# Optimization experiments

Hardware: AMD Instinct MI355X
Metric: run time of the kernel (lower is better)

## Reference

```python
import jax, jax.numpy as jnp
import numpy as np


def setup_inputs() -> dict:
    key = jax.random.key(0)
    ks = jax.random.split(key, 7)
    B = 4096
    x = jax.random.normal(ks[0], (B, 1, 28, 28), dtype=jnp.float32)
    # conv1: Conv2d(1, 32, 3), conv2: Conv2d(32, 64, 3)
    w1 = jax.random.normal(ks[1], (32, 1, 3, 3), dtype=jnp.float32) * 0.1
    b1 = jax.random.normal(ks[2], (32,), dtype=jnp.float32) * 0.1
    w2 = jax.random.normal(ks[3], (64, 32, 3, 3), dtype=jnp.float32) * 0.05
    b2 = jax.random.normal(ks[4], (64,), dtype=jnp.float32) * 0.05
    # fc1: Linear(9216, 128), fc2: Linear(128, 10)
    fc1_w = jax.random.normal(ks[5], (128, 9216), dtype=jnp.float32) * 0.01
    fc1_b = jnp.zeros((128,), dtype=jnp.float32)
    fc2_w = jax.random.normal(ks[6], (10, 128), dtype=jnp.float32) * 0.05
    fc2_b = jnp.zeros((10,), dtype=jnp.float32)
    return {"x": x, "w1": w1, "b1": b1, "w2": w2, "b2": b2,
            "fc1_w": fc1_w, "fc1_b": fc1_b, "fc2_w": fc2_w, "fc2_b": fc2_b}


def _conv_valid(x, w, b):
    # The original FFTConv1d (flatten-to-1D FFT circular correlation + roll +
    # crop) is mathematically identical to valid cross-correlation (nn.Conv2d).
    y = jax.lax.conv_general_dilated(
        x, w, window_strides=(1, 1), padding="VALID",
        dimension_numbers=("NCHW", "OIHW", "NCHW"))
    return y + b[None, :, None, None]


def reference(x, w1, b1, w2, b2, fc1_w, fc1_b, fc2_w, fc2_b):
    h = jax.nn.relu(_conv_valid(x, w1, b1))        # [B,32,26,26]
    h = jax.nn.relu(_conv_valid(h, w2, b2))        # [B,64,24,24]
    B, C, H, W = h.shape
    h = h.reshape(B, C, H // 2, 2, W // 2, 2).max(axis=(3, 5))  # maxpool 2x2 -> [B,64,12,12]
    # dropout layers are identity at inference
    h = h.reshape(B, -1)                           # [B,9216], C-major like torch.flatten
    h = jax.nn.relu(h @ fc1_w.T + fc1_b)           # [B,128]
    logits = h @ fc2_w.T + fc2_b                   # [B,10]
    # original computes log_softmax but returns the pre-softmax logits
    return logits
```

## Files before the change

### kernel.cpp

```cpp
#include <hip/hip_runtime.h>
#include <hip/hip_bf16.h>
#include <string.h>

using short8 = __attribute__((ext_vector_type(8))) short;
using f32x4  = __attribute__((ext_vector_type(4))) float;

#define POOLN     9216
#define FC1N      128
#define WT2_ELEMS 18432
#define WT2_BYTES 36864
#define H1S_STRIDE 36
#define XS_STRIDE  29

#define GLL16(gp, lp) __builtin_amdgcn_global_load_lds( \
    (const __attribute__((address_space(1))) void*)(gp), \
    (__attribute__((address_space(3))) void*)(lp), 16, 0, 0)

static __device__ __forceinline__ unsigned short f2bf(float f) {
  unsigned int u = __builtin_bit_cast(unsigned int, f);
  unsigned int r = (u + 0x7FFFu + ((u >> 16) & 1u)) >> 16;
  return (unsigned short)r;
}

static __device__ __forceinline__ unsigned int pkbf(float lo, float hi) {
  __hip_bfloat162 h2 = __float22bfloat162_rn(make_float2(lo, hi));
  unsigned int r;
  memcpy(&r, &h2, sizeof(r));
  return r;
}

__global__ __launch_bounds__(256) void k_wt2(const float* __restrict__ w2,
    unsigned short* __restrict__ wt2) {
  int idx = blockIdx.x * 256 + threadIdx.x;
  if (idx >= WT2_ELEMS) return;
  int j = idx & 7;
  int l = (idx >> 3) & 63;
  int tn = idx >> 9;
  int tap = tn >> 2, n = tn & 3;
  int oc = n * 16 + (l & 15);
  int ic = (l >> 4) * 8 + j;
  wt2[idx] = f2bf(w2[oc * 288 + ic * 9 + tap]);
}

__global__ __launch_bounds__(256) void k_fw1t(const float* __restrict__ w,
    unsigned short* __restrict__ wt) {
  int c = blockIdx.x;
  __shared__ float row[9216];
  int t = threadIdx.x;
  const float* src = w + (size_t)c * 9216;
  for (int i = t; i < 9216; i += 256) row[i] = src[i];
  __syncthreads();
  unsigned short* dst = wt + (size_t)c * 9216;
  for (int k = t; k < 9216; k += 256) {
    int sp = k >> 6, oc = k & 63;
    dst[k] = f2bf(row[oc * 144 + sp]);
  }
}

__global__ __launch_bounds__(256, 3) void kc_fused(const float* __restrict__ x,
    const float* __restrict__ w1, const float* __restrict__ b1,
    const unsigned short* __restrict__ wt2, const float* __restrict__ b2,
    unsigned short* __restrict__ pooled) {
  int img = blockIdx.x;
  int tt = blockIdx.y;
  __shared__ float xs[12 * XS_STRIDE];
  __shared__ __align__(16) unsigned short h1s[260 * H1S_STRIDE];
  int t = threadIdx.x;
  int wv = t >> 6, ln = t & 63;
  int r0x = tt * 8;

  const float* xp = x + (size_t)img * 784 + (size_t)r0x * 28;
  for (int i = t; i < 12 * 28; i += 256) {
    int r = i / 28, c = i - r * 28;
    xs[r * XS_STRIDE + c] = xp[r * 28 + c];
  }

  int wvu = __builtin_amdgcn_readfirstlane(wv);
  float wr[8][9], br[8];
  #pragma unroll
  for (int o = 0; o < 8; ++o) {
    br[o] = b1[wvu * 8 + o];
    #pragma unroll
    for (int q = 0; q < 9; ++q) wr[o][q] = w1[(wvu * 8 + o) * 9 + q];
  }
  __syncthreads();

  if (ln < 52) {
    int half = (ln >= 26);
    int xcol = ln - half * 26;
    int y0 = half * 5;
    float win[3][3];
    #pragma unroll
    for (int c = 0; c < 3; ++c) {
      win[1][c] = xs[(y0 + 0) * XS_STRIDE + xcol + c];
      win[2][c] = xs[(y0 + 1) * XS_STRIDE + xcol + c];
    }
    #pragma unroll
    for (int i = 0; i < 5; ++i) {
      #pragma unroll
      for (int c = 0; c < 3; ++c) {
        win[0][c] = win[1][c];
        win[1][c] = win[2][c];
        win[2][c] = xs[(y0 + i + 2) * XS_STRIDE + xcol + c];
      }
      unsigned int packed[4];
      #pragma unroll
      for (int o = 0; o < 8; o += 2) {
        float s0 = br[o], s1 = br[o + 1];
        #pragma unroll
        for (int r = 0; r < 3; ++r)
          #pragma unroll
          for (int c = 0; c < 3; ++c) {
            s0 = fmaf(win[r][c], wr[o][r * 3 + c], s0);
            s1 = fmaf(win[r][c], wr[o + 1][r * 3 + c], s1);
          }
        packed[o >> 1] = pkbf(fmaxf(s0, 0.f), fmaxf(s1, 0.f));
      }
      int pos = (y0 + i) * 26 + xcol;
      unsigned short* dst = &h1s[pos * H1S_STRIDE + wv * 8];
      *(uint2*)dst = make_uint2(packed[0], packed[1]);
      *(uint2*)(dst + 4) = make_uint2(packed[2], packed[3]);
    }
  }
  __syncthreads();

  int col = ln & 15;
  int g = (ln >> 4) & 3;

  int abase[3];
  #pragma unroll
  for (int i = 0; i < 3; ++i) {
    int y = 2 * wv + (col & 1);
    int xx = 8 * i + (col >> 1);
    abase[i] = (y * 26 + xx) * (H1S_STRIDE * 2) + g * 16;
  }

  f32x4 acc[3][4];
  #pragma unroll
  for (int m = 0; m < 3; ++m)
    #pragma unroll
    for (int n = 0; n < 4; ++n)
      acc[m][n] = (f32x4){0.f, 0.f, 0.f, 0.f};

  const char* hsb = (const char*)h1s;
  #pragma unroll
  for (int tap = 0; tap < 9; ++tap) {
    int ky = tap / 3, kx = tap - ky * 3;
    int toff = (ky * 26 + kx) * (H1S_STRIDE * 2);
    short8 bf[4];
    #pragma unroll
    for (int n = 0; n < 4; ++n)
      bf[n] = *(const short8*)(wt2 + ((size_t)(tap * 4 + n) * 64 + ln) * 8);
    #pragma unroll
    for (int m = 0; m < 3; ++m) {
      union { short8 v; uint2 d[2]; } af;
      af.d[0] = *(const uint2*)(hsb + abase[m] + toff);
      af.d[1] = *(const uint2*)(hsb + abase[m] + toff + 8);
      #pragma unroll
      for (int n = 0; n < 4; ++n)
        acc[m][n] = __builtin_amdgcn_mfma_f32_16x16x32_bf16(af.v, bf[n], acc[m][n], 0, 0, 0);
    }
  }

  float bias[4];
  #pragma unroll
  for (int n = 0; n < 4; ++n) bias[n] = b2[n * 16 + col];
  unsigned short* pp = pooled + (size_t)img * POOLN;
  int pr = tt * 4 + wv;
  #pragma unroll
  for (int m = 0; m < 3; ++m) {
    int sp = pr * 12 + m * 4 + g;
    float rv[4];
    #pragma unroll
    for (int n = 0; n < 4; ++n) {
      f32x4 a = acc[m][n];
      float v = fmaxf(fmaxf(a[0], a[1]), fmaxf(a[2], a[3]));
      rv[n] = fmaxf(v + bias[n], 0.f);
    }
    unsigned int p01 = pkbf(rv[0], rv[1]);
    unsigned int p23 = pkbf(rv[2], rv[3]);
    unsigned short* pr0 = pp + sp * 64 + col;
    pr0[0]  = (unsigned short)p01;
    pr0[16] = (unsigned short)(p01 >> 16);
    pr0[32] = (unsigned short)p23;
    pr0[48] = (unsigned short)(p23 >> 16);
  }
}

__global__ __launch_bounds__(256) void k3_fc1_mfma(
    const unsigned short* __restrict__ a, const unsigned short* __restrict__ w,
    float* __restrict__ part, int nrpad) {
  __shared__ __align__(16) unsigned short As[2][4096];
  __shared__ __align__(16) unsigned short Bs[2][8192];
  int row0 = blockIdx.x * 64;
  int kbase = blockIdx.y * 2304;
  int t = threadIdx.x;
  int wv = t >> 6, l = t & 63;
  int rsub = l >> 3;
  int src_sw = ((l & 7) ^ rsub) << 4;

  const char* abase = (const char*)a + (size_t)row0 * 18432;
  const char* bbase = (const char*)w;

  auto stage = [&](int buf, int step) {
    size_t k0b = (size_t)(kbase + step * 64) * 2;
    #pragma unroll
    for (int i = 0; i < 2; ++i) {
      int c = wv * 2 + i;
      GLL16(abase + (size_t)(c * 8 + rsub) * 18432 + k0b + src_sw,
            (char*)As[buf] + c * 1024);
    }
    #pragma unroll
    for (int i = 0; i < 4; ++i) {
      int c = wv * 4 + i;
      GLL16(bbase + (size_t)(c * 8 + rsub) * 18432 + k0b + src_sw,
            (char*)Bs[buf] + c * 1024);
    }
  };

  int wm = wv >> 1, wn = wv & 1;
  int lr = l & 15, g2 = l >> 4;
  int rdxor = (lr & 7) << 4;

  f32x4 acc[2][4];
  #pragma unroll
  for (int mf = 0; mf < 2; ++mf)
    #pragma unroll
    for (int nf = 0; nf < 4; ++nf)
      acc[mf][nf] = (f32x4){0.f, 0.f, 0.f, 0.f};

  stage(0, 0);
  __syncthreads();
  for (int s = 0; s < 36; ++s) {
    int cur = s & 1;
    if (s < 35) stage(cur ^ 1, s + 1);
    const char* Ab = (const char*)As[cur];
    const char* Bb = (const char*)Bs[cur];
    #pragma unroll
    for (int ksub = 0; ksub < 2; ++ksub) {
      int koff = (ksub * 64 + g2 * 16) ^ rdxor;
      short8 af0 = *(const short8*)(Ab + (wm * 32 + lr) * 128 + koff);
      short8 af1 = *(const short8*)(Ab + (wm * 32 + 16 + lr) * 128 + koff);
      short8 bf[4];
      #pragma unroll
      for (int nf = 0; nf < 4; ++nf)
        bf[nf] = *(const short8*)(Bb + (wn * 64 + nf * 16 + lr) * 128 + koff);
      #pragma unroll
      for (int nf = 0; nf < 4; ++nf) {
        acc[0][nf] = __builtin_amdgcn_mfma_f32_16x16x32_bf16(af0, bf[nf], acc[0][nf], 0, 0, 0);
        acc[1][nf] = __builtin_amdgcn_mfma_f32_16x16x32_bf16(af1, bf[nf], acc[1][nf], 0, 0, 0);
      }
    }
    __syncthreads();
  }

  float* pp = part + (size_t)blockIdx.y * nrpad * 128 + (size_t)row0 * 128;
  #pragma unroll
  for (int mf = 0; mf < 2; ++mf)
    #pragma unroll
    for (int nf = 0; nf < 4; ++nf)
      #pragma unroll
      for (int rr = 0; rr < 4; ++rr) {
        int r = wm * 32 + mf * 16 + g2 * 4 + rr;
        int c = wn * 64 + nf * 16 + lr;
        pp[r * 128 + c] = acc[mf][nf][rr];
      }
}

__global__ __launch_bounds__(256) void k_red(const float* __restrict__ part,
    const float* __restrict__ bias, float* __restrict__ f1o, int nr, int nrpad) {
  int i = blockIdx.x * 256 + threadIdx.x;
  if (i >= nr * 128) return;
  size_t stride = (size_t)nrpad * 128;
  float s = part[i] + part[stride + i] + part[2 * stride + i] + part[3 * stride + i];
  f1o[i] = fmaxf(s + bias[i & 127], 0.f);
}

__global__ __launch_bounds__(256) void k4_fc2(const float* __restrict__ h,
    const float* __restrict__ w, const float* __restrict__ bias,
    float* __restrict__ out, int nr) {
  int idx = blockIdx.x * 256 + threadIdx.x;
  if (idx >= nr * 10) return;
  int b = idx / 10;
  int j = idx - b * 10;
  const float4* hp = (const float4*)(h + (size_t)b * 128);
  const float4* wp = (const float4*)(w + (size_t)j * 128);
  float s = 0.f;
  #pragma unroll
  for (int q = 0; q < 32; ++q) {
    float4 hv = hp[q];
    float4 wv = wp[q];
    s = fmaf(hv.x, wv.x, s);
    s = fmaf(hv.y, wv.y, s);
    s = fmaf(hv.z, wv.z, s);
    s = fmaf(hv.w, wv.w, s);
  }
  out[idx] = s + bias[j];
}

extern "C" void kernel_launch(void* const* d_in, const int* in_sizes, int n_in,
                              void* d_out, int out_size, void* d_ws, size_t ws_size,
                              hipStream_t stream) {
  const float* x   = (const float*)d_in[0];
  const float* w1  = (const float*)d_in[1];
  const float* b1  = (const float*)d_in[2];
  const float* w2  = (const float*)d_in[3];
  const float* b2  = (const float*)d_in[4];
  const float* fw1 = (const float*)d_in[5];
  const float* fb1 = (const float*)d_in[6];
  const float* fw2 = (const float*)d_in[7];
  const float* fb2 = (const float*)d_in[8];
  float* out = (float*)d_out;

  const int B = in_sizes[0] / 784;

  unsigned short* wt2 = (unsigned short*)d_ws;
  unsigned short* fw1t = (unsigned short*)((char*)d_ws + WT2_BYTES);
  const size_t carve = WT2_BYTES + (size_t)9216 * 128 * 2;
  char* base = (char*)d_ws + carve;
  size_t avail = (ws_size > carve) ? ws_size - carve : 0;
  const size_t per_img = (size_t)POOLN * 2 + 512 + 2048;
  int Bc = (int)(avail / per_img);
  if (Bc > B) Bc = B;
  Bc &= ~63;
  if (Bc < 64) Bc = 64;

  unsigned short* pooled = (unsigned short*)base;
  float* f1o = (float*)(base + (size_t)Bc * (POOLN * 2));
  float* part = (float*)(base + (size_t)Bc * (POOLN * 2 + 512));

  k_wt2<<<(WT2_ELEMS + 255) / 256, 256, 0, stream>>>(w2, wt2);
  k_fw1t<<<128, 256, 0, stream>>>(fw1, fw1t);

  for (int i0 = 0; i0 < B; i0 += Bc) {
    int nr = (B - i0 < Bc) ? (B - i0) : Bc;
    int mtiles = (nr + 63) / 64;
    int nrpad = mtiles * 64;
    kc_fused<<<dim3(nr, 3), 256, 0, stream>>>(x + (size_t)i0 * 784, w1, b1,
                                              wt2, b2, pooled);
    k3_fc1_mfma<<<dim3(mtiles, 4), 256, 0, stream>>>(pooled, fw1t, part, nrpad);
    k_red<<<(nr * 128 + 255) / 256, 256, 0, stream>>>(part, fb1, f1o, nr, nrpad);
    k4_fc2<<<(nr * 10 + 255) / 256, 256, 0, stream>>>(f1o, fw2, fb2,
                                                      out + (size_t)i0 * 10, nr);
  }
}
```

Before: 157.9 us.

## Fuse fc1 reduction with fc2, pack conv1 FMAs, raise conv occupancy

After: 156.0 us. About the same (-1.2%).

```diff
diff --git a/kernel.cpp b/kernel.cpp
--- a/kernel.cpp
+++ b/kernel.cpp
@@ -4,6 +4,7 @@
 
 using short8 = __attribute__((ext_vector_type(8))) short;
 using f32x4  = __attribute__((ext_vector_type(4))) float;
+using f32x2  = __attribute__((ext_vector_type(2))) float;
 
 #define POOLN     9216
 #define FC1N      128
@@ -57,7 +58,7 @@
   }
 }
 
-__global__ __launch_bounds__(256, 3) void kc_fused(const float* __restrict__ x,
+__global__ __launch_bounds__(256, 4) void kc_fused(const float* __restrict__ x,
     const float* __restrict__ w1, const float* __restrict__ b1,
     const unsigned short* __restrict__ wt2, const float* __restrict__ b2,
     unsigned short* __restrict__ pooled) {
@@ -76,12 +77,14 @@
   }
 
   int wvu = __builtin_amdgcn_readfirstlane(wv);
-  float wr[8][9], br[8];
-  #pragma unroll
-  for (int o = 0; o < 8; ++o) {
-    br[o] = b1[wvu * 8 + o];
-    #pragma unroll
-    for (int q = 0; q < 9; ++q) wr[o][q] = w1[(wvu * 8 + o) * 9 + q];
+  f32x2 wp[4][9], bp[4];
+  #pragma unroll
+  for (int p = 0; p < 4; ++p) {
+    int o = wvu * 8 + p * 2;
+    bp[p] = (f32x2){b1[o], b1[o + 1]};
+    #pragma unroll
+    for (int q = 0; q < 9; ++q)
+      wp[p][q] = (f32x2){w1[o * 9 + q], w1[(o + 1) * 9 + q]};
   }
   __syncthreads();
 
@@ -103,18 +106,22 @@
         win[1][c] = win[2][c];
         win[2][c] = xs[(y0 + i + 2) * XS_STRIDE + xcol + c];
       }
+      f32x2 s[4] = {bp[0], bp[1], bp[2], bp[3]};
+      #pragma unroll
+      for (int r = 0; r < 3; ++r)
+        #pragma unroll
+        for (int c = 0; c < 3; ++c) {
+          f32x2 wv2 = (f32x2){win[r][c], win[r][c]};
+          #pragma unroll
+          for (int p = 0; p < 4; ++p)
+            s[p] = __builtin_elementwise_fma(wv2, wp[p][r * 3 + c], s[p]);
+        }
       unsigned int packed[4];
-      #pragma unroll
-      for (int o = 0; o < 8; o += 2) {
-        float s0 = br[o], s1 = br[o + 1];
-        #pragma unroll
-        for (int r = 0; r < 3; ++r)
-          #pragma unroll
-          for (int c = 0; c < 3; ++c) {
-            s0 = fmaf(win[r][c], wr[o][r * 3 + c], s0);
-            s1 = fmaf(win[r][c], wr[o + 1][r * 3 + c], s1);
-          }
-        packed[o >> 1] = pkbf(fmaxf(s0, 0.f), fmaxf(s1, 0.f));
+      const f32x2 z2 = (f32x2){0.f, 0.f};
+      #pragma unroll
+      for (int p = 0; p < 4; ++p) {
+        f32x2 sp = __builtin_elementwise_max(s[p], z2);
+        packed[p] = pkbf(sp.x, sp.y);
       }
       int pos = (y0 + i) * 26 + xcol;
       unsigned short* dst = &h1s[pos * H1S_STRIDE + wv * 8];
@@ -267,35 +274,40 @@
       }
 }
 
-__global__ __launch_bounds__(256) void k_red(const float* __restrict__ part,
-    const float* __restrict__ bias, float* __restrict__ f1o, int nr, int nrpad) {
-  int i = blockIdx.x * 256 + threadIdx.x;
-  if (i >= nr * 128) return;
+__global__ __launch_bounds__(256) void k_tail(const float* __restrict__ part,
+    const float* __restrict__ fb1, const float* __restrict__ fw2,
+    const float* __restrict__ fb2, float* __restrict__ out,
+    int nr, int nrpad) {
+  __shared__ float sh[2][128];
+  int t = threadIdx.x;
+  int r = t >> 7, c = t & 127;
+  int row = blockIdx.x * 2 + r;
   size_t stride = (size_t)nrpad * 128;
-  float s = part[i] + part[stride + i] + part[2 * stride + i] + part[3 * stride + i];
-  f1o[i] = fmaxf(s + bias[i & 127], 0.f);
-}
-
-__global__ __launch_bounds__(256) void k4_fc2(const float* __restrict__ h,
-    const float* __restrict__ w, const float* __restrict__ bias,
-    float* __restrict__ out, int nr) {
-  int idx = blockIdx.x * 256 + threadIdx.x;
-  if (idx >= nr * 10) return;
-  int b = idx / 10;
-  int j = idx - b * 10;
-  const float4* hp = (const float4*)(h + (size_t)b * 128);
-  const float4* wp = (const float4*)(w + (size_t)j * 128);
-  float s = 0.f;
-  #pragma unroll
-  for (int q = 0; q < 32; ++q) {
-    float4 hv = hp[q];
-    float4 wv = wp[q];
-    s = fmaf(hv.x, wv.x, s);
-    s = fmaf(hv.y, wv.y, s);
-    s = fmaf(hv.z, wv.z, s);
-    s = fmaf(hv.w, wv.w, s);
-  }
-  out[idx] = s + bias[j];
+  if (row < nr) {
+    size_t i = (size_t)row * 128 + c;
+    float s = part[i] + part[stride + i] + part[2 * stride + i] + part[3 * stride + i];
+    sh[r][c] = fmaxf(s + fb1[c], 0.f);
+  }
+  __syncthreads();
+  if (t < 20) {
+    int rr = t / 10, j = t - rr * 10;
+    int orow = blockIdx.x * 2 + rr;
+    if (orow < nr) {
+      const float4* hv = (const float4*)sh[rr];
+      const float4* wv = (const float4*)(fw2 + (size_t)j * 128);
+      float s = 0.f;
+      #pragma unroll
+      for (int q = 0; q < 32; ++q) {
+        float4 h4 = hv[q];
+        float4 w4 = wv[q];
+        s = fmaf(h4.x, w4.x, s);
+        s = fmaf(h4.y, w4.y, s);
+        s = fmaf(h4.z, w4.z, s);
+        s = fmaf(h4.w, w4.w, s);
+      }
+      out[(size_t)orow * 10 + j] = s + fb2[j];
+    }
+  }
 }
 
 extern "C" void kernel_launch(void* const* d_in, const int* in_sizes, int n_in,
@@ -319,15 +331,14 @@
   const size_t carve = WT2_BYTES + (size_t)9216 * 128 * 2;
   char* base = (char*)d_ws + carve;
   size_t avail = (ws_size > carve) ? ws_size - carve : 0;
-  const size_t per_img = (size_t)POOLN * 2 + 512 + 2048;
+  const size_t per_img = (size_t)POOLN * 2 + 2048;
   int Bc = (int)(avail / per_img);
   if (Bc > B) Bc = B;
   Bc &= ~63;
   if (Bc < 64) Bc = 64;
 
   unsigned short* pooled = (unsigned short*)base;
-  float* f1o = (float*)(base + (size_t)Bc * (POOLN * 2));
-  float* part = (float*)(base + (size_t)Bc * (POOLN * 2 + 512));
+  float* part = (float*)(base + (size_t)Bc * (POOLN * 2));
 
   k_wt2<<<(WT2_ELEMS + 255) / 256, 256, 0, stream>>>(w2, wt2);
   k_fw1t<<<128, 256, 0, stream>>>(fw1, fw1t);
@@ -339,8 +350,7 @@
     kc_fused<<<dim3(nr, 3), 256, 0, stream>>>(x + (size_t)i0 * 784, w1, b1,
                                               wt2, b2, pooled);
     k3_fc1_mfma<<<dim3(mtiles, 4), 256, 0, stream>>>(pooled, fw1t, part, nrpad);
-    k_red<<<(nr * 128 + 255) / 256, 256, 0, stream>>>(part, fb1, f1o, nr, nrpad);
-    k4_fc2<<<(nr * 10 + 255) / 256, 256, 0, stream>>>(f1o, fw2, fb2,
-                                                      out + (size_t)i0 * 10, nr);
-  }
-}
+    k_tail<<<(nr + 1) / 2, 256, 0, stream>>>(part, fb1, fw2, fb2,
+                                             out + (size_t)i0 * 10, nr, nrpad);
+  }
+}
```
